# Optimization experiments

Hardware: AMD Instinct MI355X
Metric: run time of the kernel (lower is better)

## Reference

```python
import jax, jax.numpy as jnp
import numpy as np

IH, IW = 256, 704
FH, FW = 32, 88
D_MIN, D_MAX, D_RES = 1.0, 60.0, 0.5
D = int(np.ceil((D_MAX - D_MIN) / D_RES))  # 118 depth bins
C_IN, HID, C_OUT = 256, 64, 80
N_R, N_THETA = 128, 256
BN_EPS = 1e-5


def _edges():
    # non-uniform polar grid: angular bins uniform, radial bins grow with r
    ang = np.linspace(-np.pi / 2, np.pi / 2, N_THETA + 1).astype(np.float32)
    t = np.linspace(0.0, 1.0, N_R + 1)
    rad = (D_MIN + (t ** 1.5) * (D_MAX - D_MIN)).astype(np.float32)
    return jnp.asarray(ang), jnp.asarray(rad)


def _frustum():
    # [D, fH, fW, 3] of (u, v, depth) samples in image space
    ds = np.arange(D_MIN, D_MAX, D_RES, dtype=np.float32)
    xs = np.linspace(0, IW - 1, FW, dtype=np.float32)
    ys = np.linspace(0, IH - 1, FH, dtype=np.float32)
    d = np.broadcast_to(ds[:, None, None], (D, FH, FW))
    x = np.broadcast_to(xs[None, None, :], (D, FH, FW))
    y = np.broadcast_to(ys[None, :, None], (D, FH, FW))
    return jnp.asarray(np.stack([x, y, d], axis=-1))


def _bn(x, g, b, m, v):
    # inference-mode BatchNorm2d over channel axis 1; x: [BN, C, H, W]
    inv = g / jnp.sqrt(v + BN_EPS)
    return x * inv[None, :, None, None] + (b - m * inv)[None, :, None, None]


def setup_inputs() -> dict:
    key = jax.random.key(0)
    ks = jax.random.split(key, 8)
    B, N = 2, 1
    x = jax.random.normal(ks[0], (B, N, C_IN, FH, FW), dtype=jnp.float32)
    # camera->lidar axis permutation: x_l = z_c, y_l = -x_c, z_l = -y_c
    R = jnp.asarray([[0.0, 0.0, 1.0], [-1.0, 0.0, 0.0], [0.0, -1.0, 0.0]], dtype=jnp.float32)
    camera2lidar_rots = jnp.broadcast_to(R, (B, N, 3, 3))
    camera2lidar_trans = jnp.zeros((B, N, 3), dtype=jnp.float32)
    K = jnp.asarray([[380.0, 0.0, IW / 2.0], [0.0, 380.0, IH / 2.0], [0.0, 0.0, 1.0]], dtype=jnp.float32)
    intrins = jnp.broadcast_to(K, (B, N, 3, 3))
    s = 0.02
    params = dict(
        w1=jax.random.normal(ks[1], (HID, C_IN), dtype=jnp.float32) * s,
        b1=jnp.zeros((HID,), dtype=jnp.float32),
        g1=jnp.ones((HID,), dtype=jnp.float32),
        be1=jnp.zeros((HID,), dtype=jnp.float32),
        m1=jax.random.normal(ks[2], (HID,), dtype=jnp.float32) * s,
        v1=jnp.abs(jax.random.normal(ks[3], (HID,), dtype=jnp.float32)) + 0.5,
        w2=jax.random.normal(ks[4], (D + C_OUT, HID), dtype=jnp.float32) * s,
        b2=jnp.zeros((D + C_OUT,), dtype=jnp.float32),
        g2=jnp.ones((D + C_OUT,), dtype=jnp.float32),
        be2=jnp.zeros((D + C_OUT,), dtype=jnp.float32),
        m2=jax.random.normal(ks[5], (D + C_OUT,), dtype=jnp.float32) * s,
        v2=jnp.abs(jax.random.normal(ks[6], (D + C_OUT,), dtype=jnp.float32)) + 0.5,
    )
    return dict(x=x, camera2lidar_rots=camera2lidar_rots,
                camera2lidar_trans=camera2lidar_trans, intrins=intrins, **params)


def reference(x, camera2lidar_rots, camera2lidar_trans, intrins,
              w1, b1, g1, be1, m1, v1, w2, b2, g2, be2, m2, v2):
    B, N = x.shape[0], x.shape[1]
    # --- LIFT: DepthNet (two 1x1 convs + BN) -> depth dist x features outer product ---
    xf = x.reshape(B * N, C_IN, FH, FW)
    h = jnp.einsum('bchw,oc->bohw', xf, w1) + b1[None, :, None, None]
    h = jax.nn.relu(_bn(h, g1, be1, m1, v1))
    h = jnp.einsum('bchw,oc->bohw', h, w2) + b2[None, :, None, None]
    h = _bn(h, g2, be2, m2, v2)
    depth = jax.nn.softmax(h[:, :D], axis=1)            # [BN, D, fH, fW]
    feat = h[:, D:D + C_OUT]                            # [BN, C, fH, fW]
    lifted = depth[:, None, :, :, :] * feat[:, :, None, :, :]   # [BN, C, D, fH, fW]
    lifted = lifted.reshape(B, N, C_OUT, D, FH, FW).transpose(0, 1, 3, 4, 5, 2)  # [B,N,D,fH,fW,C]

    # --- geometry: unproject frustum to lidar frame ---
    fr = _frustum()                                      # [D, fH, fW, 3]
    u, v_, d = fr[..., 0], fr[..., 1], fr[..., 2]
    fx = intrins[..., 0, 0][:, :, None, None, None]
    fy = intrins[..., 1, 1][:, :, None, None, None]
    cx = intrins[..., 0, 2][:, :, None, None, None]
    cy = intrins[..., 1, 2][:, :, None, None, None]
    pc = jnp.stack([(u - cx) * d / fx, (v_ - cy) * d / fy,
                    jnp.broadcast_to(d, (B, N, D, FH, FW))], axis=-1)  # [B,N,D,fH,fW,3]
    pts = jnp.einsum('bnij,bndhwj->bndhwi', camera2lidar_rots, pc)
    pts = pts + camera2lidar_trans[:, :, None, None, None, :]

    # --- SPLAT: scatter-sum into non-uniform polar BEV grid ---
    ang_e, rad_e = _edges()
    xl, yl = pts[..., 0], pts[..., 1]
    r = jnp.sqrt(xl * xl + yl * yl)
    th = jnp.arctan2(yl, xl)
    r_idx = jnp.searchsorted(rad_e, r, side='right') - 1   # non-uniform bins -> bucketize
    t_idx = jnp.searchsorted(ang_e, th, side='right') - 1
    valid = (r_idx >= 0) & (r_idx < N_R) & (t_idx >= 0) & (t_idx < N_THETA)
    b_idx = jnp.arange(B)[:, None, None, None, None]
    trash = B * N_R * N_THETA  # dummy segment for out-of-grid points
    seg = jnp.where(valid, (b_idx * N_R + r_idx) * N_THETA + t_idx, trash).reshape(-1)
    bev = jax.ops.segment_sum(lifted.reshape(-1, C_OUT), seg, num_segments=trash + 1)[:-1]
    bev = bev.reshape(B, N_R, N_THETA, C_OUT).transpose(0, 3, 1, 2)  # [B, C, n_r, n_theta]
    return bev
```

## Files before the change

### kernel.cpp

```cpp
#include <hip/hip_runtime.h>
#include <hip/hip_bf16.h>
#include <hip/hip_cooperative_groups.h>
#include <math.h>

namespace cg = cooperative_groups;

#define FH 32
#define FW 88
#define DD 118
#define C_IN 256
#define HID 64
#define C_OUT 80
#define NPIX 5632
#define PIX_PER_B 2816
#define N_R 128
#define N_THETA 256
#define NCOL 176
#define NBIN 32768
#define ECAP 12
#define PSTRIDE 9440

#define FRONT_MLP  352
#define FRONT_BINS 82
#define FRONT_ZERO 320
#define FRONT_TOTAL (FRONT_MLP + FRONT_BINS + FRONT_ZERO)

typedef __attribute__((ext_vector_type(8))) short short8;
typedef __attribute__((ext_vector_type(4))) float f32x4;

__device__ inline float bf2f(unsigned short h) {
  return __uint_as_float((unsigned)h << 16);
}
__device__ inline unsigned short f2bf(float f) {
  unsigned u = __float_as_uint(f);
  unsigned r = (u + 0x7fffu + ((u >> 16) & 1u)) >> 16;
  return (unsigned short)r;
}
__device__ inline bool detect_bf16(const void* intr) {
  float f = __uint_as_float(*(const unsigned*)intr);
  return !(f > 300.0f && f < 500.0f);
}
__device__ inline float ldf(const void* p, int i, bool isb) {
  return isb ? bf2f(((const unsigned short*)p)[i]) : ((const float*)p)[i];
}

__device__ inline void load_geom(int tid, float* radEL, float* angEL, float* camsL,
                                 const void* rots, const void* trans, const void* intr,
                                 bool isb) {
  if (tid < 129) {
    double t = (double)tid * (1.0 / 128.0);
    radEL[tid] = (float)(1.0 + pow(t, 1.5) * 59.0);
  }
  for (int i = tid; i < 257; i += 256) {
    double step = M_PI / 256.0;
    double vv = (i == 256) ? (M_PI / 2.0) : ((double)i * step + (-M_PI / 2.0));
    angEL[i] = (float)vv;
  }
  if (tid < 18) camsL[tid] = ldf(rots, tid, isb);
  if (tid < 6)  camsL[20 + tid] = ldf(trans, tid, isb);
  if (tid >= 6 && tid < 24) camsL[28 + (tid - 6)] = ldf(intr, tid - 6, isb);
}

__device__ inline int computeBin(int w, int h, int d,
                                 const float* camsF, int b,
                                 const float* radE, const float* angE) {
  float fx = camsF[28 + b * 9 + 0], cx = camsF[28 + b * 9 + 2];
  float fy = camsF[28 + b * 9 + 4], cy = camsF[28 + b * 9 + 5];
  float R00 = camsF[b * 9 + 0], R01 = camsF[b * 9 + 1], R02 = camsF[b * 9 + 2];
  float R10 = camsF[b * 9 + 3], R11 = camsF[b * 9 + 4], R12 = camsF[b * 9 + 5];
  float Tx = camsF[20 + b * 3 + 0], Ty = camsF[20 + b * 3 + 1];
  float u  = (w == FW - 1) ? 703.0f : (float)((double)w * (703.0 / 87.0));
  float vv = (h == FH - 1) ? 255.0f : (float)((double)h * (255.0 / 31.0));
  float dd = 1.0f + 0.5f * (float)d;
  float px = __fdiv_rn(__fmul_rn(__fsub_rn(u, cx), dd), fx);
  float py = __fdiv_rn(__fmul_rn(__fsub_rn(vv, cy), dd), fy);
  float xl = __fadd_rn(__fadd_rn(__fadd_rn(__fmul_rn(R00, px), __fmul_rn(R01, py)),
                                 __fmul_rn(R02, dd)), Tx);
  float yl = __fadd_rn(__fadd_rn(__fadd_rn(__fmul_rn(R10, px), __fmul_rn(R11, py)),
                                 __fmul_rn(R12, dd)), Ty);
  float r = __fsqrt_rn(__fadd_rn(__fmul_rn(xl, xl), __fmul_rn(yl, yl)));
  float th = (float)atan2((double)yl, (double)xl);
  int lo = 0, hi = 129;
  while (lo < hi) { int mid = (lo + hi) >> 1; if (radE[mid] <= r) lo = mid + 1; else hi = mid; }
  int ri = lo - 1;
  lo = 0; hi = 257;
  while (lo < hi) { int mid = (lo + hi) >> 1; if (angE[mid] <= th) lo = mid + 1; else hi = mid; }
  int ti = lo - 1;
  bool valid = (ri >= 0) && (ri < N_R) && (ti >= 0) && (ti < N_THETA);
  return valid ? (ri * N_THETA + ti) : -1;
}


__device__ __forceinline__ void dev_mlp(
    int pix0, int tid, float* shbuf, float* h1L,
    float* inv1L, float* b1fL, float* inv2L, float* b2fL,
    const void* __restrict__ xraw,
    const void* __restrict__ w1r, const void* __restrict__ b1r,
    const void* __restrict__ g1r, const void* __restrict__ be1r,
    const void* __restrict__ m1r, const void* __restrict__ v1r,
    const void* __restrict__ w2r, const void* __restrict__ b2r,
    const void* __restrict__ g2r, const void* __restrict__ be2r,
    const void* __restrict__ m2r, const void* __restrict__ v2r,
    float* __restrict__ depthW, float* __restrict__ featW, bool isb) {
  unsigned short* xsU = (unsigned short*)shbuf;
  float* h2s = shbuf;
  float* smaxL = shbuf + 3200;
  float* ssumL = shbuf + 3456;
  if (tid < 64) {
    float iv = ldf(g1r, tid, isb) / sqrtf(ldf(v1r, tid, isb) + 1e-5f);
    inv1L[tid] = iv;
    b1fL[tid] = ldf(b1r, tid, isb) * iv + (ldf(be1r, tid, isb) - ldf(m1r, tid, isb) * iv);
  }
  if (tid < 198) {
    float iv = ldf(g2r, tid, isb) / sqrtf(ldf(v2r, tid, isb) + 1e-5f);
    inv2L[tid] = iv;
    b2fL[tid] = ldf(b2r, tid, isb) * iv + (ldf(be2r, tid, isb) - ldf(m2r, tid, isb) * iv);
  }
  int b = pix0 / PIX_PER_B;
  int ploc0 = pix0 - b * PIX_PER_B;
  size_t xbase = (size_t)b * C_IN * PIX_PER_B + ploc0;
  const unsigned short* xh = (const unsigned short*)xraw;
  const float* xf = (const float*)xraw;
  {
    int p = tid & 15, crow = tid >> 4;
    for (int it = 0; it < 16; it++) {
      int c = it * 16 + crow;
      size_t gi = xbase + (size_t)c * PIX_PER_B + p;
      xsU[p * 264 + c] = isb ? xh[gi] : f2bf(xf[gi]);
    }
  }
  int lane = tid & 63, wv = tid >> 6;
  int nloc = lane & 15, quad = lane >> 4;
  int orow = wv * 16 + nloc;
  short8 afr[8];
  const unsigned short* w1h = (const unsigned short*)w1r;
  const float* w1f32 = (const float*)w1r;
  if (isb) {
#pragma unroll
    for (int s = 0; s < 8; s++)
      afr[s] = *(const short8*)(w1h + orow * 256 + s * 32 + quad * 8);
  } else {
#pragma unroll
    for (int s = 0; s < 8; s++) {
      short8 a;
#pragma unroll
      for (int j = 0; j < 8; j++)
        a[j] = (short)f2bf(w1f32[orow * 256 + s * 32 + quad * 8 + j]);
      afr[s] = a;
    }
  }
  __syncthreads();
  f32x4 acc = {0.f, 0.f, 0.f, 0.f};
#pragma unroll
  for (int s = 0; s < 8; s++) {
    short8 bfr = *(const short8*)(xsU + nloc * 264 + s * 32 + quad * 8);
    acc = __builtin_amdgcn_mfma_f32_16x16x32_bf16(afr[s], bfr, acc, 0, 0, 0);
  }
#pragma unroll
  for (int r = 0; r < 4; r++) {
    int mm = wv * 16 + quad * 4 + r;
    float hv = fmaxf(fmaf(acc[r], inv1L[mm], b1fL[mm]), 0.f);
    h1L[nloc * 68 + mm] = hv;
  }
  __syncthreads();
  int p = tid & 15, g = tid >> 4;
  float h1v[64];
  const float4* hp = (const float4*)(h1L + p * 68);
#pragma unroll
  for (int k4 = 0; k4 < 16; k4++) {
    float4 hv = hp[k4];
    h1v[4 * k4 + 0] = hv.x; h1v[4 * k4 + 1] = hv.y;
    h1v[4 * k4 + 2] = hv.z; h1v[4 * k4 + 3] = hv.w;
  }
  for (int j = 0; j < 13; j++) {
    int o = g * 13 + j;
    if (o < 198) {
      float iv = inv2L[o];
      float accs = b2fL[o];
      if (isb) {
        const ushort4* wr = (const ushort4*)w2r;
#pragma unroll
        for (int k4 = 0; k4 < 16; k4++) {
          ushort4 uw = wr[o * 16 + k4];
          accs = fmaf(bf2f(uw.x) * iv, h1v[4 * k4 + 0], accs);
          accs = fmaf(bf2f(uw.y) * iv, h1v[4 * k4 + 1], accs);
          accs = fmaf(bf2f(uw.z) * iv, h1v[4 * k4 + 2], accs);
          accs = fmaf(bf2f(uw.w) * iv, h1v[4 * k4 + 3], accs);
        }
      } else {
        const float4* wr = (const float4*)w2r;
#pragma unroll
        for (int k4 = 0; k4 < 16; k4++) {
          float4 w = wr[o * 16 + k4];
          accs = fmaf(w.x * iv, h1v[4 * k4 + 0], accs);
          accs = fmaf(w.y * iv, h1v[4 * k4 + 1], accs);
          accs = fmaf(w.z * iv, h1v[4 * k4 + 2], accs);
          accs = fmaf(w.w * iv, h1v[4 * k4 + 3], accs);
        }
      }
      h2s[o * 16 + p] = accs;
    }
  }
  __syncthreads();
  int r0 = g * 8, r1 = min(118, r0 + 8);
  float lm = -INFINITY;
  for (int o = r0; o < r1; o++) lm = fmaxf(lm, h2s[o * 16 + p]);
  smaxL[g * 16 + p] = lm;
  __syncthreads();
  float m = smaxL[p];
#pragma unroll
  for (int gg = 1; gg < 16; gg++) m = fmaxf(m, smaxL[gg * 16 + p]);
  float ls = 0.f;
  for (int o = r0; o < r1; o++) ls += expf(h2s[o * 16 + p] - m);
  ssumL[g * 16 + p] = ls;
  __syncthreads();
  float tot = 0.f;
#pragma unroll
  for (int gg = 0; gg < 16; gg++) tot += ssumL[gg * 16 + p];
  int pix = pix0 + p;
  for (int o = r0; o < r1; o++)
    depthW[(size_t)pix * DD + o] = expf(h2s[o * 16 + p] - m) / tot;
  int f0 = g * 5;
  for (int f = f0; f < f0 + 5; f++)
    featW[(size_t)pix * C_OUT + f] = h2s[(118 + f) * 16 + p];
}

__device__ __forceinline__ void dev_bins(
    int blk_rel, int tid, float* radEL, float* angEL, float* camsL,
    const void* rots, const void* trans, const void* intr, bool isb,
    int* __restrict__ cnt, unsigned* __restrict__ ent, int* __restrict__ flag) {
  int t = blk_rel * 256 + tid;
  load_geom(tid, radEL, angEL, camsL, rots, trans, intr, isb);
  __syncthreads();
  if (t < NCOL * DD) {
    int col = t / DD, d = t - col * DD;
    int b = col / FW, w = col - b * FW;
    float R01 = camsL[b * 9 + 1], R11 = camsL[b * 9 + 4];
    if (!(R01 == 0.0f && R11 == 0.0f)) atomicOr(flag, 1);
    int bin = computeBin(w, 0, d, camsL, b, radEL, angEL);
    if (bin >= 0) {
      int slot = atomicAdd(&cnt[b * NBIN + bin], 1);
      if (slot < ECAP) ent[(size_t)(b * NBIN + bin) * ECAP + slot] = ((unsigned)col << 8) | (unsigned)d;
      else atomicOr(flag, 1);
    }
  }
}

__device__ __forceinline__ void dev_pcol(
    int col, int tid, float* depthL, float* featL,
    const float* __restrict__ depthW, const float* __restrict__ featW,
    float* __restrict__ P) {
  int b = col / FW, w = col - b * FW;
  size_t colPix = (size_t)b * PIX_PER_B + w;
  for (int i = tid; i < FH * DD; i += 256) {
    int h = i / DD, d = i - h * DD;
    depthL[d * 33 + h] = depthW[(colPix + (size_t)h * FW) * DD + d];
  }
  for (int i = tid; i < FH * C_OUT; i += 256) {
    int h = i / C_OUT, c = i - h * C_OUT;
    featL[i] = featW[(colPix + (size_t)h * FW) * C_OUT + c];
  }
  __syncthreads();
  const float4* featL4 = (const float4*)featL;
  float4* P4 = (float4*)(P + (size_t)col * PSTRIDE);
  for (int t = tid; t < DD * 20; t += 256) {
    int d = t / 20, c4 = t - d * 20;
    float4 a = make_float4(0.f, 0.f, 0.f, 0.f);
#pragma unroll
    for (int h = 0; h < FH; h++) {
      float wd = depthL[d * 33 + h];
      float4 f = featL4[h * 20 + c4];
      a.x = fmaf(wd, f.x, a.x); a.y = fmaf(wd, f.y, a.y);
      a.z = fmaf(wd, f.z, a.z); a.w = fmaf(wd, f.w, a.w);
    }
    P4[d * 20 + c4] = a;
  }
}

__device__ __forceinline__ void dev_scatter(
    int idx2, int tid, float* depthL, float* featL,
    float* radEL, float* angEL, float* camsL,
    const void* rots, const void* trans, const void* intr, bool isb,
    const float* __restrict__ depthW, const float* __restrict__ featW,
    float* __restrict__ bevAcc) {
  int col = idx2 >> 1, chalf = idx2 & 1;
  int b = col / FW, w = col - b * FW;
  load_geom(tid, radEL, angEL, camsL, rots, trans, intr, isb);
  size_t colPix = (size_t)b * PIX_PER_B + w;
  for (int i = tid; i < FH * DD; i += 256) {
    int h = i / DD, d = i - h * DD;
    depthL[d * 33 + h] = depthW[(colPix + (size_t)h * FW) * DD + d];
  }
  for (int i = tid; i < FH * C_OUT; i += 256) {
    int h = i / C_OUT, c = i - h * C_OUT;
    featL[i] = featW[(colPix + (size_t)h * FW) * C_OUT + c];
  }
  __syncthreads();
  const float4* featL4 = (const float4*)featL;
  for (int t = tid; t < DD * FH * 10; t += 256) {
    int d = t / 320, rem = t - d * 320;
    int h = rem / 10, c4 = chalf * 10 + (rem - (rem / 10) * 10);
    int bin = computeBin(w, h, d, camsL, b, radEL, angEL);
    if (bin < 0) continue;
    float wd = depthL[d * 33 + h];
    float4 f = featL4[h * 20 + c4];
    float* outb = bevAcc + (((size_t)(b * C_OUT + c4 * 4)) << 15) + bin;
    unsafeAtomicAdd(outb, wd * f.x);
    unsafeAtomicAdd(outb + (1u << 15), wd * f.y);
    unsafeAtomicAdd(outb + (2u << 15), wd * f.z);
    unsafeAtomicAdd(outb + (3u << 15), wd * f.w);
  }
}

__device__ __forceinline__ void dev_out_main(
    int vt, int tid, const float* __restrict__ P,
    const int* __restrict__ cnt, const unsigned* __restrict__ ent,
    void* __restrict__ out, bool isb) {
  int b = vt >> 9;
  int ri = (vt >> 2) & 127;
  int q = vt & 3;
  int ti = tid;
  int bin = ri * N_THETA + ti;
  int n = cnt[b * NBIN + bin];
  if (n > ECAP) n = ECAP;
  unsigned ee[ECAP];
  const unsigned* eb = ent + (size_t)(b * NBIN + bin) * ECAP;
  for (int i = 0; i < n; i++) ee[i] = eb[i];
  for (int i = 1; i < n; i++) {
    unsigned key = ee[i]; int j = i - 1;
    while (j >= 0 && ee[j] > key) { ee[j + 1] = ee[j]; j--; }
    ee[j + 1] = key;
  }
  int base[ECAP];
  for (int i = 0; i < n; i++)
    base[i] = (int)(((ee[i] >> 8) * PSTRIDE + (ee[i] & 255u) * C_OUT) >> 2);
  const float4* P4 = (const float4*)P;
  unsigned short* oh = (unsigned short*)out;
  float* of = (float*)out;
  size_t obase = (((size_t)(b * C_OUT)) << 15) + bin;
  for (int c4 = q * 5; c4 < q * 5 + 5; c4++) {
    float4 s = make_float4(0.f, 0.f, 0.f, 0.f);
    for (int i = 0; i < n; i++) {
      float4 v = P4[base[i] + c4];
      s.x += v.x; s.y += v.y; s.z += v.z; s.w += v.w;
    }
    size_t o0 = obase + ((size_t)(c4 * 4) << 15);
    if (isb) {
      oh[o0]              = f2bf(s.x);
      oh[o0 + (1u << 15)] = f2bf(s.y);
      oh[o0 + (2u << 15)] = f2bf(s.z);
      oh[o0 + (3u << 15)] = f2bf(s.w);
    } else {
      of[o0]              = s.x;
      of[o0 + (1u << 15)] = s.y;
      of[o0 + (2u << 15)] = s.z;
      of[o0 + (3u << 15)] = s.w;
    }
  }
}

__device__ __forceinline__ void dev_out_copy(
    int gtid, int gstride, const float* __restrict__ bevAcc,
    void* __restrict__ out, bool isb) {
  const float4* a4 = (const float4*)bevAcc;
  int n4 = (NBIN * 2 * C_OUT) / 4;
  if (isb) {
    ushort4* o4 = (ushort4*)out;
    for (int i = gtid; i < n4; i += gstride) {
      float4 v = a4[i];
      ushort4 o; o.x = f2bf(v.x); o.y = f2bf(v.y); o.z = f2bf(v.z); o.w = f2bf(v.w);
      o4[i] = o;
    }
  } else {
    float4* o4 = (float4*)out;
    for (int i = gtid; i < n4; i += gstride) o4[i] = a4[i];
  }
}

__global__ __launch_bounds__(256) void k_fused(
    const void* __restrict__ xraw,
    const void* __restrict__ rots, const void* __restrict__ trans,
    const void* __restrict__ intr,
    const void* __restrict__ w1r, const void* __restrict__ b1r,
    const void* __restrict__ g1r, const void* __restrict__ be1r,
    const void* __restrict__ m1r, const void* __restrict__ v1r,
    const void* __restrict__ w2r, const void* __restrict__ b2r,
    const void* __restrict__ g2r, const void* __restrict__ be2r,
    const void* __restrict__ m2r, const void* __restrict__ v2r,
    int* __restrict__ cnt, unsigned* __restrict__ ent, int* __restrict__ flag,
    float* __restrict__ depthW, float* __restrict__ featW,
    float* __restrict__ bevAcc, float* __restrict__ P, void* __restrict__ out) {
  __shared__ __align__(16) float SH[6464];
  __shared__ float inv1L[64], b1fL[64], inv2L[198], b2fL[198];
  __shared__ float radEL[129], angEL[257], camsL[46];
  cg::grid_group grid = cg::this_grid();
  int tid = threadIdx.x;
  int bid = blockIdx.x, nb = gridDim.x;
  bool isb = detect_bf16(intr);

  for (int i = bid * 256 + tid; i < NBIN * 2 + 64; i += nb * 256) cnt[i] = 0;
  grid.sync();

  for (int vb = bid; vb < FRONT_MLP + FRONT_BINS; vb += nb) {
    if (vb < FRONT_MLP) {
      dev_mlp(vb * 16, tid, SH, SH + 3712, inv1L, b1fL, inv2L, b2fL,
              xraw, w1r, b1r, g1r, be1r, m1r, v1r,
              w2r, b2r, g2r, be2r, m2r, v2r, depthW, featW, isb);
    } else {
      dev_bins(vb - FRONT_MLP, tid, radEL, angEL, camsL,
               rots, trans, intr, isb, cnt, ent, flag);
    }
    __syncthreads();
  }
  grid.sync();

  int fl = *(volatile int*)flag;
  if (fl == 0) {
    for (int col = bid; col < NCOL; col += nb) {
      dev_pcol(col, tid, SH, SH + 3896, depthW, featW, P);
      __syncthreads();
    }
    grid.sync();
    for (int vt = bid; vt < 1024; vt += nb)
      dev_out_main(vt, tid, P, cnt, ent, out, isb);
  } else {
    float4 z = make_float4(0.f, 0.f, 0.f, 0.f);
    float4* bz = (float4*)bevAcc;
    int n4 = (NBIN * 2 * C_OUT) / 4;
    for (int i = bid * 256 + tid; i < n4; i += nb * 256) bz[i] = z;
    grid.sync();
    for (int vt = bid; vt < NCOL * 2; vt += nb) {
      dev_scatter(vt, tid, SH, SH + 3896, radEL, angEL, camsL,
                  rots, trans, intr, isb, depthW, featW, bevAcc);
      __syncthreads();
    }
    grid.sync();
    dev_out_copy(bid * 256 + tid, nb * 256, bevAcc, out, isb);
  }
}

__global__ __launch_bounds__(256) void k_front(
    const void* __restrict__ xraw,
    const void* __restrict__ rots, const void* __restrict__ trans,
    const void* __restrict__ intr,
    const void* __restrict__ w1r, const void* __restrict__ b1r,
    const void* __restrict__ g1r, const void* __restrict__ be1r,
    const void* __restrict__ m1r, const void* __restrict__ v1r,
    const void* __restrict__ w2r, const void* __restrict__ b2r,
    const void* __restrict__ g2r, const void* __restrict__ be2r,
    const void* __restrict__ m2r, const void* __restrict__ v2r,
    int* __restrict__ cnt, unsigned* __restrict__ ent, int* __restrict__ flag,
    float* __restrict__ depthW, float* __restrict__ featW,
    float* __restrict__ bevAcc) {
  __shared__ __align__(16) float shbuf[3712];
  __shared__ __align__(16) float h1L[16 * 68];
  __shared__ float inv1L[64], b1fL[64], inv2L[198], b2fL[198];
  __shared__ float radEL[129], angEL[257], camsL[46];
  int tid = threadIdx.x;
  bool isb = detect_bf16(intr);
  if (blockIdx.x >= FRONT_MLP + FRONT_BINS) {
    int zb = blockIdx.x - (FRONT_MLP + FRONT_BINS);
    float4 z = make_float4(0.f, 0.f, 0.f, 0.f);
    float4* bz = (float4*)bevAcc;
    int n4 = (NBIN * 2 * C_OUT) / 4;
    for (int i = zb * 256 + tid; i < n4; i += FRONT_ZERO * 256) bz[i] = z;
    return;
  }
  if (blockIdx.x >= FRONT_MLP) {
    dev_bins(blockIdx.x - FRONT_MLP, tid, radEL, angEL, camsL,
             rots, trans, intr, isb, cnt, ent, flag);
    return;
  }
  dev_mlp(blockIdx.x * 16, tid, shbuf, h1L, inv1L, b1fL, inv2L, b2fL,
          xraw, w1r, b1r, g1r, be1r, m1r, v1r,
          w2r, b2r, g2r, be2r, m2r, v2r, depthW, featW, isb);
}

__global__ __launch_bounds__(256) void k_back(const float* __restrict__ depthW,
                                              const float* __restrict__ featW,
                                              const int* __restrict__ flag,
                                              const void* __restrict__ rots,
                                              const void* __restrict__ trans,
                                              const void* __restrict__ intr,
                                              float* __restrict__ P,
                                              float* __restrict__ bevAcc) {
  __shared__ float depthL[DD * 33];
  __shared__ __align__(16) float featL[FH * C_OUT];
  __shared__ float radEL[129], angEL[257], camsL[46];
  __shared__ int flagS;
  int tid = threadIdx.x;
  if (tid == 0) flagS = *flag;
  __syncthreads();
  if (blockIdx.x < NCOL) {
    if (flagS != 0) return;
    dev_pcol(blockIdx.x, tid, depthL, featL, depthW, featW, P);
    return;
  }
  if (flagS == 0) return;
  bool isb = detect_bf16(intr);
  dev_scatter(blockIdx.x - NCOL, tid, depthL, featL, radEL, angEL, camsL,
              rots, trans, intr, isb, depthW, featW, bevAcc);
}

__global__ __launch_bounds__(256) void k_out(const float* __restrict__ P,
                                             const int* __restrict__ cnt,
                                             const unsigned* __restrict__ ent,
                                             const int* __restrict__ flag,
                                             const float* __restrict__ bevAcc,
                                             void* __restrict__ out,
                                             const void* __restrict__ intrRaw) {
  bool isb = detect_bf16(intrRaw);
  int tid = threadIdx.x;
  if (*flag != 0) {
    dev_out_copy(blockIdx.x * 256 + tid, 1024 * 256, bevAcc, out, isb);
    return;
  }
  dev_out_main(blockIdx.x, tid, P, cnt, ent, out, isb);
}

extern "C" void kernel_launch(void* const* d_in, const int* in_sizes, int n_in,
                              void* d_out, int out_size, void* d_ws, size_t ws_size,
                              hipStream_t stream) {
  const void* x     = d_in[0];
  const void* rots  = d_in[1];
  const void* trans = d_in[2];
  const void* intr  = d_in[3];
  const void* w1  = d_in[4];
  const void* b1  = d_in[5];
  const void* g1  = d_in[6];
  const void* be1 = d_in[7];
  const void* m1  = d_in[8];
  const void* v1  = d_in[9];
  const void* w2  = d_in[10];
  const void* b2  = d_in[11];
  const void* g2  = d_in[12];
  const void* be2 = d_in[13];
  const void* m2  = d_in[14];
  const void* v2  = d_in[15];

  float* ws = (float*)d_ws;
  float*    P      = ws + 0;
  int*      cnt    = (int*)(ws + 1661440);
  int*      flag   = (int*)(ws + 1726976);
  unsigned* ent    = (unsigned*)(ws + 1727040);
  float*    depthW = ws + 2513472;
  float*    featW  = ws + 3178048;
  float*    bevAcc = ws + 3628608;

  static int gblk = -2;
  if (gblk == -2) {
    int dev = 0;
    (void)hipGetDevice(&dev);
    int coop = 0, numCU = 0, maxb = 0;
    (void)hipDeviceGetAttribute(&coop, hipDeviceAttributeCooperativeLaunch, dev);
    (void)hipDeviceGetAttribute(&numCU, hipDeviceAttributeMultiprocessorCount, dev);
    hipError_t e = hipOccupancyMaxActiveBlocksPerMultiprocessor(&maxb, (const void*)k_fused, 256, 0);
    if (coop && e == hipSuccess && numCU > 0 && maxb > 0) {
      long g = (long)maxb * (long)numCU;
      gblk = (int)(g > 512 ? 512 : g);
    } else {
      gblk = -1;
    }
  }

  if (gblk > 0) {
    void* ka[24] = { (void*)&x, (void*)&rots, (void*)&trans, (void*)&intr,
                     (void*)&w1, (void*)&b1, (void*)&g1, (void*)&be1,
                     (void*)&m1, (void*)&v1, (void*)&w2, (void*)&b2,
                     (void*)&g2, (void*)&be2, (void*)&m2, (void*)&v2,
                     (void*)&cnt, (void*)&ent, (void*)&flag,
                     (void*)&depthW, (void*)&featW, (void*)&bevAcc,
                     (void*)&P, (void*)&d_out };
    hipError_t e = hipLaunchCooperativeKernel((const void*)k_fused, dim3(gblk), dim3(256),
                                              ka, 0u, stream);
    if (e == hipSuccess) return;
    gblk = -1;
  }

  (void)hipMemsetAsync(cnt, 0, (size_t)(65536 + 64) * sizeof(int), stream);
  k_front<<<FRONT_TOTAL, 256, 0, stream>>>(x, rots, trans, intr,
                                           w1, b1, g1, be1, m1, v1,
                                           w2, b2, g2, be2, m2, v2,
                                           cnt, ent, flag, depthW, featW, bevAcc);
  k_back<<<NCOL * 3, 256, 0, stream>>>(depthW, featW, flag, rots, trans, intr, P, bevAcc);
  k_out<<<1024, 256, 0, stream>>>(P, cnt, ent, flag, bevAcc, d_out, intr);
}
```

Before: 142.7 us.

## Register-block P-column and MLP loops, widen out blocks, move cnt zeroing to memset

The second MLP layer now uses four independent accumulators to break the FMA dependency chain. The depth-feature column product is register-blocked over four depth bins, with depth stored h-major so it can be read as float4. The output gather gives each block all 20 channel groups instead of a quarter, which cuts the block count from 1024 to 256. The counter zeroing and its grid.sync move out of the cooperative kernel into a host memset, and the launch tries a grid of 2x the CU count when occupancy allows. Changing the grid size affects load balance, and doing more work per thread raises register pressure.

```diff
diff --git a/kernel.cpp b/kernel.cpp
--- a/kernel.cpp
+++ b/kernel.cpp
@@ -176,29 +176,59 @@
     int o = g * 13 + j;
     if (o < 198) {
       float iv = inv2L[o];
-      float accs = b2fL[o];
+      float q0 = 0.f, q1 = 0.f, q2 = 0.f, q3 = 0.f;
       if (isb) {
         const ushort4* wr = (const ushort4*)w2r;
 #pragma unroll
-        for (int k4 = 0; k4 < 16; k4++) {
-          ushort4 uw = wr[o * 16 + k4];
-          accs = fmaf(bf2f(uw.x) * iv, h1v[4 * k4 + 0], accs);
-          accs = fmaf(bf2f(uw.y) * iv, h1v[4 * k4 + 1], accs);
-          accs = fmaf(bf2f(uw.z) * iv, h1v[4 * k4 + 2], accs);
-          accs = fmaf(bf2f(uw.w) * iv, h1v[4 * k4 + 3], accs);
+        for (int k4 = 0; k4 < 16; k4 += 4) {
+          ushort4 u0 = wr[o * 16 + k4 + 0];
+          ushort4 u1 = wr[o * 16 + k4 + 1];
+          ushort4 u2 = wr[o * 16 + k4 + 2];
+          ushort4 u3 = wr[o * 16 + k4 + 3];
+          q0 = fmaf(bf2f(u0.x) * iv, h1v[4 * k4 + 0], q0);
+          q0 = fmaf(bf2f(u0.y) * iv, h1v[4 * k4 + 1], q0);
+          q0 = fmaf(bf2f(u0.z) * iv, h1v[4 * k4 + 2], q0);
+          q0 = fmaf(bf2f(u0.w) * iv, h1v[4 * k4 + 3], q0);
+          q1 = fmaf(bf2f(u1.x) * iv, h1v[4 * k4 + 4], q1);
+          q1 = fmaf(bf2f(u1.y) * iv, h1v[4 * k4 + 5], q1);
+          q1 = fmaf(bf2f(u1.z) * iv, h1v[4 * k4 + 6], q1);
+          q1 = fmaf(bf2f(u1.w) * iv, h1v[4 * k4 + 7], q1);
+          q2 = fmaf(bf2f(u2.x) * iv, h1v[4 * k4 + 8], q2);
+          q2 = fmaf(bf2f(u2.y) * iv, h1v[4 * k4 + 9], q2);
+          q2 = fmaf(bf2f(u2.z) * iv, h1v[4 * k4 + 10], q2);
+          q2 = fmaf(bf2f(u2.w) * iv, h1v[4 * k4 + 11], q2);
+          q3 = fmaf(bf2f(u3.x) * iv, h1v[4 * k4 + 12], q3);
+          q3 = fmaf(bf2f(u3.y) * iv, h1v[4 * k4 + 13], q3);
+          q3 = fmaf(bf2f(u3.z) * iv, h1v[4 * k4 + 14], q3);
+          q3 = fmaf(bf2f(u3.w) * iv, h1v[4 * k4 + 15], q3);
         }
       } else {
         const float4* wr = (const float4*)w2r;
 #pragma unroll
-        for (int k4 = 0; k4 < 16; k4++) {
-          float4 w = wr[o * 16 + k4];
-          accs = fmaf(w.x * iv, h1v[4 * k4 + 0], accs);
-          accs = fmaf(w.y * iv, h1v[4 * k4 + 1], accs);
-          accs = fmaf(w.z * iv, h1v[4 * k4 + 2], accs);
-          accs = fmaf(w.w * iv, h1v[4 * k4 + 3], accs);
+        for (int k4 = 0; k4 < 16; k4 += 4) {
+          float4 w0 = wr[o * 16 + k4 + 0];
+          float4 w1v = wr[o * 16 + k4 + 1];
+          float4 w2v = wr[o * 16 + k4 + 2];
+          float4 w3v = wr[o * 16 + k4 + 3];
+          q0 = fmaf(w0.x * iv, h1v[4 * k4 + 0], q0);
+          q0 = fmaf(w0.y * iv, h1v[4 * k4 + 1], q0);
+          q0 = fmaf(w0.z * iv, h1v[4 * k4 + 2], q0);
+          q0 = fmaf(w0.w * iv, h1v[4 * k4 + 3], q0);
+          q1 = fmaf(w1v.x * iv, h1v[4 * k4 + 4], q1);
+          q1 = fmaf(w1v.y * iv, h1v[4 * k4 + 5], q1);
+          q1 = fmaf(w1v.z * iv, h1v[4 * k4 + 6], q1);
+          q1 = fmaf(w1v.w * iv, h1v[4 * k4 + 7], q1);
+          q2 = fmaf(w2v.x * iv, h1v[4 * k4 + 8], q2);
+          q2 = fmaf(w2v.y * iv, h1v[4 * k4 + 9], q2);
+          q2 = fmaf(w2v.z * iv, h1v[4 * k4 + 10], q2);
+          q2 = fmaf(w2v.w * iv, h1v[4 * k4 + 11], q2);
+          q3 = fmaf(w3v.x * iv, h1v[4 * k4 + 12], q3);
+          q3 = fmaf(w3v.y * iv, h1v[4 * k4 + 13], q3);
+          q3 = fmaf(w3v.z * iv, h1v[4 * k4 + 14], q3);
+          q3 = fmaf(w3v.w * iv, h1v[4 * k4 + 15], q3);
         }
       }
-      h2s[o * 16 + p] = accs;
+      h2s[o * 16 + p] = b2fL[o] + ((q0 + q1) + (q2 + q3));
     }
   }
   __syncthreads();
@@ -254,7 +284,7 @@
   size_t colPix = (size_t)b * PIX_PER_B + w;
   for (int i = tid; i < FH * DD; i += 256) {
     int h = i / DD, d = i - h * DD;
-    depthL[d * 33 + h] = depthW[(colPix + (size_t)h * FW) * DD + d];
+    depthL[h * 120 + d] = depthW[(colPix + (size_t)h * FW) * DD + d];
   }
   for (int i = tid; i < FH * C_OUT; i += 256) {
     int h = i / C_OUT, c = i - h * C_OUT;
@@ -262,18 +292,34 @@
   }
   __syncthreads();
   const float4* featL4 = (const float4*)featL;
+  const float4* depthL4 = (const float4*)depthL;
   float4* P4 = (float4*)(P + (size_t)col * PSTRIDE);
-  for (int t = tid; t < DD * 20; t += 256) {
-    int d = t / 20, c4 = t - d * 20;
-    float4 a = make_float4(0.f, 0.f, 0.f, 0.f);
+  for (int t = tid; t < 30 * 20; t += 256) {
+    int dq = t / 20, c4 = t - dq * 20;
+    float4 a0 = make_float4(0.f, 0.f, 0.f, 0.f);
+    float4 a1 = make_float4(0.f, 0.f, 0.f, 0.f);
+    float4 a2 = make_float4(0.f, 0.f, 0.f, 0.f);
+    float4 a3 = make_float4(0.f, 0.f, 0.f, 0.f);
 #pragma unroll
     for (int h = 0; h < FH; h++) {
-      float wd = depthL[d * 33 + h];
+      float4 wd = depthL4[h * 30 + dq];
       float4 f = featL4[h * 20 + c4];
-      a.x = fmaf(wd, f.x, a.x); a.y = fmaf(wd, f.y, a.y);
-      a.z = fmaf(wd, f.z, a.z); a.w = fmaf(wd, f.w, a.w);
-    }
-    P4[d * 20 + c4] = a;
+      a0.x = fmaf(wd.x, f.x, a0.x); a0.y = fmaf(wd.x, f.y, a0.y);
+      a0.z = fmaf(wd.x, f.z, a0.z); a0.w = fmaf(wd.x, f.w, a0.w);
+      a1.x = fmaf(wd.y, f.x, a1.x); a1.y = fmaf(wd.y, f.y, a1.y);
+      a1.z = fmaf(wd.y, f.z, a1.z); a1.w = fmaf(wd.y, f.w, a1.w);
+      a2.x = fmaf(wd.z, f.x, a2.x); a2.y = fmaf(wd.z, f.y, a2.y);
+      a2.z = fmaf(wd.z, f.z, a2.z); a2.w = fmaf(wd.z, f.w, a2.w);
+      a3.x = fmaf(wd.w, f.x, a3.x); a3.y = fmaf(wd.w, f.y, a3.y);
+      a3.z = fmaf(wd.w, f.z, a3.z); a3.w = fmaf(wd.w, f.w, a3.w);
+    }
+    int d0 = dq * 4;
+    P4[(d0 + 0) * 20 + c4] = a0;
+    P4[(d0 + 1) * 20 + c4] = a1;
+    if (d0 + 2 < DD) {
+      P4[(d0 + 2) * 20 + c4] = a2;
+      P4[(d0 + 3) * 20 + c4] = a3;
+    }
   }
 }
 
@@ -316,11 +362,9 @@
     int vt, int tid, const float* __restrict__ P,
     const int* __restrict__ cnt, const unsigned* __restrict__ ent,
     void* __restrict__ out, bool isb) {
-  int b = vt >> 9;
-  int ri = (vt >> 2) & 127;
-  int q = vt & 3;
-  int ti = tid;
-  int bin = ri * N_THETA + ti;
+  int b = vt >> 7;
+  int ri = vt & 127;
+  int bin = ri * N_THETA + tid;
   int n = cnt[b * NBIN + bin];
   if (n > ECAP) n = ECAP;
   unsigned ee[ECAP];
@@ -338,7 +382,7 @@
   unsigned short* oh = (unsigned short*)out;
   float* of = (float*)out;
   size_t obase = (((size_t)(b * C_OUT)) << 15) + bin;
-  for (int c4 = q * 5; c4 < q * 5 + 5; c4++) {
+  for (int c4 = 0; c4 < 20; c4++) {
     float4 s = make_float4(0.f, 0.f, 0.f, 0.f);
     for (int i = 0; i < n; i++) {
       float4 v = P4[base[i] + c4];
@@ -398,9 +442,6 @@
   int bid = blockIdx.x, nb = gridDim.x;
   bool isb = detect_bf16(intr);
 
-  for (int i = bid * 256 + tid; i < NBIN * 2 + 64; i += nb * 256) cnt[i] = 0;
-  grid.sync();
-
   for (int vb = bid; vb < FRONT_MLP + FRONT_BINS; vb += nb) {
     if (vb < FRONT_MLP) {
       dev_mlp(vb * 16, tid, SH, SH + 3712, inv1L, b1fL, inv2L, b2fL,
@@ -417,11 +458,11 @@
   int fl = *(volatile int*)flag;
   if (fl == 0) {
     for (int col = bid; col < NCOL; col += nb) {
-      dev_pcol(col, tid, SH, SH + 3896, depthW, featW, P);
+      dev_pcol(col, tid, SH, SH + 3840, depthW, featW, P);
       __syncthreads();
     }
     grid.sync();
-    for (int vt = bid; vt < 1024; vt += nb)
+    for (int vt = bid; vt < 2 * N_R; vt += nb)
       dev_out_main(vt, tid, P, cnt, ent, out, isb);
   } else {
     float4 z = make_float4(0.f, 0.f, 0.f, 0.f);
@@ -484,7 +525,7 @@
                                               const void* __restrict__ intr,
                                               float* __restrict__ P,
                                               float* __restrict__ bevAcc) {
-  __shared__ float depthL[DD * 33];
+  __shared__ __align__(16) float depthL[DD * 33];
   __shared__ __align__(16) float featL[FH * C_OUT];
   __shared__ float radEL[129], angEL[257], camsL[46];
   __shared__ int flagS;
@@ -515,7 +556,8 @@
     dev_out_copy(blockIdx.x * 256 + tid, 1024 * 256, bevAcc, out, isb);
     return;
   }
-  dev_out_main(blockIdx.x, tid, P, cnt, ent, out, isb);
+  if (blockIdx.x < 2 * N_R)
+    dev_out_main(blockIdx.x, tid, P, cnt, ent, out, isb);
 }
 
 extern "C" void kernel_launch(void* const* d_in, const int* in_sizes, int n_in,
@@ -547,23 +589,31 @@
   float*    featW  = ws + 3178048;
   float*    bevAcc = ws + 3628608;
 
-  static int gblk = -2;
-  if (gblk == -2) {
+  static int g_init = 0;
+  static int g_safe = -1;
+  static int g_want = 0;
+  if (!g_init) {
+    g_init = 1;
     int dev = 0;
     (void)hipGetDevice(&dev);
     int coop = 0, numCU = 0, maxb = 0;
     (void)hipDeviceGetAttribute(&coop, hipDeviceAttributeCooperativeLaunch, dev);
     (void)hipDeviceGetAttribute(&numCU, hipDeviceAttributeMultiprocessorCount, dev);
     hipError_t e = hipOccupancyMaxActiveBlocksPerMultiprocessor(&maxb, (const void*)k_fused, 256, 0);
-    if (coop && e == hipSuccess && numCU > 0 && maxb > 0) {
-      long g = (long)maxb * (long)numCU;
-      gblk = (int)(g > 512 ? 512 : g);
+    if (coop && numCU > 0) {
+      int cap = (e == hipSuccess && maxb > 0) ? maxb : 1;
+      long s = (long)cap * (long)numCU;
+      g_safe = (int)(s > 512 ? 512 : s);
+      int w = 2 * numCU; if (w > 512) w = 512;
+      g_want = (w > g_safe) ? w : 0;
     } else {
-      gblk = -1;
-    }
-  }
-
-  if (gblk > 0) {
+      g_safe = -1;
+    }
+  }
+
+  (void)hipMemsetAsync(cnt, 0, (size_t)(65536 + 64) * sizeof(int), stream);
+
+  if (g_safe > 0) {
     void* ka[24] = { (void*)&x, (void*)&rots, (void*)&trans, (void*)&intr,
                      (void*)&w1, (void*)&b1, (void*)&g1, (void*)&be1,
                      (void*)&m1, (void*)&v1, (void*)&w2, (void*)&b2,
@@ -571,13 +621,24 @@
                      (void*)&cnt, (void*)&ent, (void*)&flag,
                      (void*)&depthW, (void*)&featW, (void*)&bevAcc,
                      (void*)&P, (void*)&d_out };
-    hipError_t e = hipLaunchCooperativeKernel((const void*)k_fused, dim3(gblk), dim3(256),
-                                              ka, 0u, stream);
+    if (g_want > 0) {
+      hipStreamCaptureStatus cs = hipStreamCaptureStatusNone;
+      hipError_t qe = hipStreamIsCapturing(stream, &cs);
+      if (qe == hipSuccess && cs == hipStreamCaptureStatusNone) {
+        hipError_t e = hipLaunchCooperativeKernel((const void*)k_fused, dim3(g_want),
+                                                  dim3(256), ka, 0u, stream);
+        if (e == hipSuccess) { g_safe = g_want; g_want = 0; return; }
+        (void)hipGetLastError();
+        g_want = 0;
+      }
+    }
+    hipError_t e = hipLaunchCooperativeKernel((const void*)k_fused, dim3(g_safe),
+                                              dim3(256), ka, 0u, stream);
     if (e == hipSuccess) return;
-    gblk = -1;
-  }
-
-  (void)hipMemsetAsync(cnt, 0, (size_t)(65536 + 64) * sizeof(int), stream);
+    (void)hipGetLastError();
+    g_safe = -1;
+  }
+
   k_front<<<FRONT_TOTAL, 256, 0, stream>>>(x, rots, trans, intr,
                                            w1, b1, g1, be1, m1, v1,
                                            w2, b2, g2, be2, m2, v2,
```

After: 146.4 us. 2.6% more time.
